# Performance work log

Hardware: AMD Instinct MI355X
Metric: run time of the kernel (lower is better)

## Reference

```python
import jax, jax.numpy as jnp
import numpy as np

EPS = 1e-6
K_STEPS = 4
USE_GATING = True


def layer_norm(x, gamma, beta):
    mu = jnp.mean(x, axis=-1, keepdims=True)
    var = jnp.mean(jnp.square(x - mu), axis=-1, keepdims=True)
    return (x - mu) * jax.lax.rsqrt(var + EPS) * gamma + beta


def setup_inputs() -> dict:
    key = jax.random.key(0)
    B, L, D, H = 4, 4096, 2048, 8192
    ks = jax.random.split(key, 16)
    s = 0.02
    return {
        "x": jax.random.normal(ks[0], (B, L, D), dtype=jnp.float32),
        "in_gamma": jnp.ones((D,), jnp.float32),
        "in_beta": jnp.zeros((D,), jnp.float32),
        "agg_w": jax.random.normal(ks[1], (D, D), jnp.float32) * s,
        "agg_b": jnp.zeros((D,), jnp.float32),
        "pn_gamma": jnp.ones((D,), jnp.float32),
        "pn_beta": jnp.zeros((D,), jnp.float32),
        "d1_w": jax.random.normal(ks[2], (D, H), jnp.float32) * s,
        "d1_b": jnp.zeros((H,), jnp.float32),
        "d2_w": jax.random.normal(ks[3], (H, D), jnp.float32) * s,
        "d2_b": jnp.zeros((D,), jnp.float32),
        "bc_w": jax.random.normal(ks[4], (D, D), jnp.float32) * s,
        "bc_b": jnp.zeros((D,), jnp.float32),
        "gate_w": jax.random.normal(ks[5], (D, D), jnp.float32) * s,
        "gate_b": jnp.zeros((D,), jnp.float32),
        "out_gamma": jnp.ones((D,), jnp.float32),
        "out_beta": jnp.zeros((D,), jnp.float32),
    }


def reference(x, in_gamma, in_beta, agg_w, agg_b, pn_gamma, pn_beta,
              d1_w, d1_b, d2_w, d2_b, bc_w, bc_b, gate_w, gate_b,
              out_gamma, out_beta):
    # Input norm over the full sequence, then extract last-position summary.
    x_norm = layer_norm(x, in_gamma, in_beta)              # [B, L, D]
    thought = x_norm[:, -1, :] @ agg_w + agg_b             # [B, D]

    # Iterative pre-norm MLP thought refinement (fixed small k -> unrolled).
    for _ in range(K_STEPS):
        t = layer_norm(thought, pn_gamma, pn_beta)
        t = jax.nn.gelu(t @ d1_w + d1_b, approximate=False)
        thought = thought + (t @ d2_w + d2_b)

    # Broadcast refined thought back to every position.
    broadcast = (thought @ bc_w + bc_b)[:, None, :]        # [B, 1, D]

    if USE_GATING:
        gate = jax.nn.sigmoid(x @ gate_w + gate_b)         # [B, L, D]
        out = x + gate * broadcast
    else:
        out = x + broadcast
    return layer_norm(out, out_gamma, out_beta)
```

## Files before the change

### kernel.cpp

```cpp
#include <hip/hip_runtime.h>
#include <stdint.h>

typedef __attribute__((ext_vector_type(8))) short short8;
typedef __attribute__((ext_vector_type(4))) float f32x4;
typedef __attribute__((ext_vector_type(4))) unsigned short us4;

__device__ inline unsigned short f2bf(float f) {
    unsigned u = __float_as_uint(f);
    u = (u + 0x7FFFu + ((u >> 16) & 1u)) >> 16;
    return (unsigned short)u;
}

__device__ inline void gload_lds16(const unsigned short* g, const unsigned short* l) {
    __builtin_amdgcn_global_load_lds(
        (const __attribute__((address_space(1))) unsigned int*)(g),
        (__attribute__((address_space(3))) unsigned int*)(l),
        16, 0, 0);
}

__global__ __launch_bounds__(256) void cvt_x_kernel(const float* __restrict__ in,
                                                    unsigned short* __restrict__ out, int n4) {
    int i = blockIdx.x * 256 + threadIdx.x;
    if (i >= n4) return;
    float4 v = reinterpret_cast<const float4*>(in)[i];
    us4 o = { f2bf(v.x), f2bf(v.y), f2bf(v.z), f2bf(v.w) };
    reinterpret_cast<us4*>(out)[i] = o;
}

__global__ __launch_bounds__(256) void transpose_w_kernel(const float* __restrict__ W,
                                                          unsigned short* __restrict__ WT,
                                                          int K, int N) {
    __shared__ float tile[32][33];
    int bn = blockIdx.x * 32;
    int bk = blockIdx.y * 32;
    int tx = threadIdx.x & 31;
    int ty = threadIdx.x >> 5;
#pragma unroll
    for (int j = 0; j < 32; j += 8)
        tile[ty + j][tx] = W[(long long)(bk + ty + j) * N + bn + tx];
    __syncthreads();
#pragma unroll
    for (int j = 0; j < 32; j += 8)
        WT[(long long)(bn + ty + j) * K + bk + tx] = f2bf(tile[tx][ty + j]);
}

__device__ inline void block_reduce2(float& s, float& q) {
#pragma unroll
    for (int o = 32; o > 0; o >>= 1) {
        s += __shfl_xor(s, o, 64);
        q += __shfl_xor(q, o, 64);
    }
    __shared__ float sh[8];
    int w = threadIdx.x >> 6;
    if ((threadIdx.x & 63) == 0) { sh[w] = s; sh[4 + w] = q; }
    __syncthreads();
    s = (sh[0] + sh[1]) + (sh[2] + sh[3]);
    q = (sh[4] + sh[5]) + (sh[6] + sh[7]);
}

__global__ __launch_bounds__(256) void ln_rows_kernel(const float* __restrict__ in, long long in_stride,
                                                      float* __restrict__ out, long long out_stride,
                                                      const float* __restrict__ gamma,
                                                      const float* __restrict__ beta) {
    const float* p = in + (long long)blockIdx.x * in_stride;
    float* q = out + (long long)blockIdx.x * out_stride;
    int t = threadIdx.x;
    float4 a = reinterpret_cast<const float4*>(p)[t];
    float4 c = reinterpret_cast<const float4*>(p)[t + 256];
    float s  = (a.x + a.y) + (a.z + a.w) + (c.x + c.y) + (c.z + c.w);
    float ss = a.x*a.x + a.y*a.y + a.z*a.z + a.w*a.w
             + c.x*c.x + c.y*c.y + c.z*c.z + c.w*c.w;
    block_reduce2(s, ss);
    const float inv = 1.0f / 2048.0f;
    float mu = s * inv;
    float var = ss * inv - mu * mu;
    float rs = rsqrtf(var + 1e-6f);
    float4 g0 = reinterpret_cast<const float4*>(gamma)[t];
    float4 g1 = reinterpret_cast<const float4*>(gamma)[t + 256];
    float4 b0 = reinterpret_cast<const float4*>(beta)[t];
    float4 b1 = reinterpret_cast<const float4*>(beta)[t + 256];
    float4 o0, o1;
    o0.x = (a.x - mu) * rs * g0.x + b0.x;
    o0.y = (a.y - mu) * rs * g0.y + b0.y;
    o0.z = (a.z - mu) * rs * g0.z + b0.z;
    o0.w = (a.w - mu) * rs * g0.w + b0.w;
    o1.x = (c.x - mu) * rs * g1.x + b1.x;
    o1.y = (c.y - mu) * rs * g1.y + b1.y;
    o1.z = (c.z - mu) * rs * g1.z + b1.z;
    o1.w = (c.w - mu) * rs * g1.w + b1.w;
    reinterpret_cast<float4*>(q)[t] = o0;
    reinterpret_cast<float4*>(q)[t + 256] = o1;
}

__global__ __launch_bounds__(256) void gelu_kernel(float* __restrict__ h, int n) {
    int i = blockIdx.x * 256 + threadIdx.x;
    if (i < n) {
        float v = h[i];
        h[i] = 0.5f * v * (1.0f + erff(v * 0.70710678118654752f));
    }
}

__global__ __launch_bounds__(256) void gemv4_kernel(const float* __restrict__ in,
                                                    const float* __restrict__ W,
                                                    const float* __restrict__ bias,
                                                    float* __restrict__ out,
                                                    int K, int N, int KC) {
    const int n4 = blockIdx.x * 256 + threadIdx.x;
    const int n = n4 * 4;
    const int k0 = blockIdx.y * KC;
    const float4* W4 = reinterpret_cast<const float4*>(W);
    const float* i0 = in;
    const float* i1 = in + K;
    const float* i2 = in + 2 * K;
    const float* i3 = in + 3 * K;
    float4 a0 = {0.f, 0.f, 0.f, 0.f}, a1 = a0, a2 = a0, a3 = a0;
#pragma unroll 4
    for (int k = k0; k < k0 + KC; ++k) {
        float4 w = W4[((long long)k * N + n) >> 2];
        float c0 = i0[k], c1 = i1[k], c2 = i2[k], c3 = i3[k];
        a0.x = fmaf(c0, w.x, a0.x); a0.y = fmaf(c0, w.y, a0.y);
        a0.z = fmaf(c0, w.z, a0.z); a0.w = fmaf(c0, w.w, a0.w);
        a1.x = fmaf(c1, w.x, a1.x); a1.y = fmaf(c1, w.y, a1.y);
        a1.z = fmaf(c1, w.z, a1.z); a1.w = fmaf(c1, w.w, a1.w);
        a2.x = fmaf(c2, w.x, a2.x); a2.y = fmaf(c2, w.y, a2.y);
        a2.z = fmaf(c2, w.z, a2.z); a2.w = fmaf(c2, w.w, a2.w);
        a3.x = fmaf(c3, w.x, a3.x); a3.y = fmaf(c3, w.y, a3.y);
        a3.z = fmaf(c3, w.z, a3.z); a3.w = fmaf(c3, w.w, a3.w);
    }
    if (blockIdx.y == 0) {
        float4 b = reinterpret_cast<const float4*>(bias)[n4];
        a0.x += b.x; a0.y += b.y; a0.z += b.z; a0.w += b.w;
        a1.x += b.x; a1.y += b.y; a1.z += b.z; a1.w += b.w;
        a2.x += b.x; a2.y += b.y; a2.z += b.z; a2.w += b.w;
        a3.x += b.x; a3.y += b.y; a3.z += b.z; a3.w += b.w;
    }
    atomicAdd(&out[n + 0], a0.x); atomicAdd(&out[n + 1], a0.y);
    atomicAdd(&out[n + 2], a0.z); atomicAdd(&out[n + 3], a0.w);
    atomicAdd(&out[N + n + 0], a1.x); atomicAdd(&out[N + n + 1], a1.y);
    atomicAdd(&out[N + n + 2], a1.z); atomicAdd(&out[N + n + 3], a1.w);
    atomicAdd(&out[2 * N + n + 0], a2.x); atomicAdd(&out[2 * N + n + 1], a2.y);
    atomicAdd(&out[2 * N + n + 2], a2.z); atomicAdd(&out[2 * N + n + 3], a2.w);
    atomicAdd(&out[3 * N + n + 0], a3.x); atomicAdd(&out[3 * N + n + 1], a3.y);
    atomicAdd(&out[3 * N + n + 2], a3.z); atomicAdd(&out[3 * N + n + 3], a3.w);
}

#define BK 64
__global__ __launch_bounds__(512, 2) void gate_gemm_kernel(const unsigned short* __restrict__ A,
                                                           const unsigned short* __restrict__ BT,
                                                           const float* __restrict__ xf,
                                                           const float* __restrict__ gate_b,
                                                           const float* __restrict__ bcast,
                                                           float* __restrict__ pre,
                                                           int M, int N, int K) {
    extern __shared__ unsigned short lds[];
    const int tid = threadIdx.x;
    const int lane = tid & 63;
    const int wave = tid >> 6;
    const int wm = wave >> 2;
    const int wn = wave & 3;
    const int bm0 = blockIdx.x * 256;
    const int bn0 = blockIdx.y * 256;
    const int NT = K / BK;

    const int ch0 = wave * 64 + lane;
    const int ch1 = 512 + wave * 64 + lane;
    const int r0 = ch0 >> 3, c0s = (ch0 & 7) ^ (r0 & 7);
    const int r1 = ch1 >> 3, c1s = (ch1 & 7) ^ (r1 & 7);
    const int srcoff0 = r0 * K + c0s * 8;
    const int srcoff1 = r1 * K + c1s * 8;
    const int ldso0 = ch0 * 8;
    const int ldso1 = ch1 * 8;

    const unsigned short* Abase = A + (long long)bm0 * K;
    const unsigned short* Bbase = BT + (long long)bn0 * K;

#define STAGE_A(buf, h, t)  do { \
        const unsigned short* g = Abase + (h) * 128 * K + (t) * BK; \
        const unsigned short* d = &lds[(buf) * 16384 + (h) * 8192]; \
        gload_lds16(g + srcoff0, d + ldso0); \
        gload_lds16(g + srcoff1, d + ldso1); } while (0)
#define STAGE_B(buf, h, t)  do { \
        const unsigned short* g = Bbase + (h) * 128 * K + (t) * BK; \
        const unsigned short* d = &lds[32768 + (buf) * 16384 + (h) * 8192]; \
        gload_lds16(g + srcoff0, d + ldso0); \
        gload_lds16(g + srcoff1, d + ldso1); } while (0)

    f32x4 acc[8][4];
#pragma unroll
    for (int i = 0; i < 8; ++i)
#pragma unroll
        for (int j = 0; j < 4; ++j)
#pragma unroll
            for (int r = 0; r < 4; ++r) acc[i][j][r] = 0.f;

    const int r16 = lane & 15, kq = lane >> 4;
    const int bwrow = (wn & 1) * 64;

    STAGE_A(0, 0, 0); STAGE_A(0, 1, 0);
    STAGE_B(0, 0, 0); STAGE_B(0, 1, 0);
    asm volatile("s_waitcnt vmcnt(0)" ::: "memory");
    __builtin_amdgcn_s_barrier();

    for (int t = 0; t < NT; ++t) {
        const int p = t & 1;
        const int u = t + 1;
        const int a_base = p * 16384 + wm * 8192;
        const int b_base = 32768 + p * 16384 + (wn >> 1) * 8192;

#pragma unroll
        for (int q = 0; q < 4; ++q) {
            const int mh = (q >> 1) * 4;
            const int nh = (q & 1) * 2;
            short8 af[4][2], bf[2][2];
#pragma unroll
            for (int mi = 0; mi < 4; ++mi) {
                const int rl = (mh + mi) * 16 + r16;
#pragma unroll
                for (int kk = 0; kk < 2; ++kk)
                    af[mi][kk] = *reinterpret_cast<const short8*>(
                        &lds[a_base + rl * 64 + (((kk << 2) | kq) ^ (rl & 7)) * 8]);
            }
#pragma unroll
            for (int ni = 0; ni < 2; ++ni) {
                const int rl = bwrow + (nh + ni) * 16 + r16;
#pragma unroll
                for (int kk = 0; kk < 2; ++kk)
                    bf[ni][kk] = *reinterpret_cast<const short8*>(
                        &lds[b_base + rl * 64 + (((kk << 2) | kq) ^ (rl & 7)) * 8]);
            }
            if (q == 0 && u < NT) { STAGE_A(1 - p, 0, u); STAGE_A(1 - p, 1, u); }
            if (q == 1 && u < NT) { STAGE_B(1 - p, 0, u); STAGE_B(1 - p, 1, u); }
            __builtin_amdgcn_s_barrier();
            __builtin_amdgcn_s_setprio(1);
#pragma unroll
            for (int mi = 0; mi < 4; ++mi)
#pragma unroll
                for (int ni = 0; ni < 2; ++ni)
#pragma unroll
                    for (int kk = 0; kk < 2; ++kk)
                        acc[mh + mi][nh + ni] = __builtin_amdgcn_mfma_f32_16x16x32_bf16(
                            af[mi][kk], bf[ni][kk], acc[mh + mi][nh + ni], 0, 0, 0);
            __builtin_amdgcn_s_setprio(0);
            if (q == 3) asm volatile("s_waitcnt vmcnt(0)" ::: "memory");
            __builtin_amdgcn_s_barrier();
        }
    }

    const int bnum = bm0 >> 12;
    const float* bc_row = bcast + (long long)bnum * N;
#pragma unroll
    for (int mi = 0; mi < 8; ++mi) {
        const int row = bm0 + wm * 128 + mi * 16 + kq * 4;
#pragma unroll
        for (int ni = 0; ni < 4; ++ni) {
            const int col = bn0 + wn * 64 + ni * 16 + r16;
            const float gb = gate_b[col];
            const float bc = bc_row[col];
#pragma unroll
            for (int r = 0; r < 4; ++r) {
                const long long off = (long long)(row + r) * N + col;
                const float v = acc[mi][ni][r] + gb;
                const float g = 1.0f / (1.0f + __expf(-v));
                pre[off] = xf[off] + g * bc;
            }
        }
    }
}
#undef STAGE_A
#undef STAGE_B

extern "C" void kernel_launch(void* const* d_in, const int* in_sizes, int n_in,
                              void* d_out, int out_size, void* d_ws, size_t ws_size,
                              hipStream_t stream) {
    const float* x         = (const float*)d_in[0];
    const float* in_gamma  = (const float*)d_in[1];
    const float* in_beta   = (const float*)d_in[2];
    const float* agg_w     = (const float*)d_in[3];
    const float* agg_b     = (const float*)d_in[4];
    const float* pn_gamma  = (const float*)d_in[5];
    const float* pn_beta   = (const float*)d_in[6];
    const float* d1_w      = (const float*)d_in[7];
    const float* d1_b      = (const float*)d_in[8];
    const float* d2_w      = (const float*)d_in[9];
    const float* d2_b      = (const float*)d_in[10];
    const float* bc_w      = (const float*)d_in[11];
    const float* bc_b      = (const float*)d_in[12];
    const float* gate_w    = (const float*)d_in[13];
    const float* gate_b    = (const float*)d_in[14];
    const float* out_gamma = (const float*)d_in[15];
    const float* out_beta  = (const float*)d_in[16];

    const int B = 4, L = 4096, D = 2048, H = 8192;
    const int M = B * L;
    float* out = (float*)d_out;

    char* ws = (char*)d_ws;
    unsigned short* xb  = (unsigned short*)ws;
    unsigned short* gwT = (unsigned short*)(ws + 67108864);
    float* tln   = (float*)(ws + 75497472);
    float* tbuf  = tln + 4 * D;
    float* hbuf  = tbuf + 4 * D;
    float* bcast = hbuf + 4 * H;

    static bool attr_done = false;
    if (!attr_done) {
        hipFuncSetAttribute((const void*)gate_gemm_kernel,
                            hipFuncAttributeMaxDynamicSharedMemorySize, 131072);
        attr_done = true;
    }

    ln_rows_kernel<<<dim3(B), dim3(256), 0, stream>>>(
        x + (long long)(L - 1) * D, (long long)L * D, tln, (long long)D, in_gamma, in_beta);
    hipMemsetAsync(tbuf, 0, 4 * D * sizeof(float), stream);
    gemv4_kernel<<<dim3(D / 1024, 64), dim3(256), 0, stream>>>(tln, agg_w, agg_b, tbuf, D, D, 32);

    for (int s = 0; s < 4; ++s) {
        ln_rows_kernel<<<dim3(B), dim3(256), 0, stream>>>(
            tbuf, (long long)D, tln, (long long)D, pn_gamma, pn_beta);
        hipMemsetAsync(hbuf, 0, 4 * H * sizeof(float), stream);
        gemv4_kernel<<<dim3(H / 1024, 32), dim3(256), 0, stream>>>(tln, d1_w, d1_b, hbuf, D, H, 64);
        gelu_kernel<<<dim3(B * H / 256), dim3(256), 0, stream>>>(hbuf, B * H);
        gemv4_kernel<<<dim3(D / 1024, 128), dim3(256), 0, stream>>>(hbuf, d2_w, d2_b, tbuf, H, D, 64);
    }
    hipMemsetAsync(bcast, 0, 4 * D * sizeof(float), stream);
    gemv4_kernel<<<dim3(D / 1024, 64), dim3(256), 0, stream>>>(tbuf, bc_w, bc_b, bcast, D, D, 32);

    cvt_x_kernel<<<dim3((M * D / 4) / 256), dim3(256), 0, stream>>>(x, xb, M * D / 4);
    transpose_w_kernel<<<dim3(D / 32, D / 32), dim3(256), 0, stream>>>(gate_w, gwT, D, D);

    gate_gemm_kernel<<<dim3(M / 256, D / 256), dim3(512), 131072, stream>>>(
        xb, gwT, x, gate_b, bcast, out, M, D, D);

    ln_rows_kernel<<<dim3(M), dim3(256), 0, stream>>>(
        out, (long long)D, out, (long long)D, out_gamma, out_beta);
}
```

Before: 559.1 us.

## Fuse layernorm/GELU into GEMV prologue and switch gate GEMM to 32x32 MFMA

Folds the per-row layernorm and the GELU into a templated GEMV kernel that stages normalized or activated inputs in LDS, which removes separate ln and gelu launches from the serial refinement chain. Each GEMV block redundantly recomputes row statistics over the full K. Separately, the large gate GEMM switches from 16x16x32 to 32x32x16 bf16 MFMA with a reorganized fragment layout and epilogue. A barrier is also added in block_reduce2 so the shared scratch can be reused safely across repeated calls.

```diff
diff --git a/kernel.cpp b/kernel.cpp
--- a/kernel.cpp
+++ b/kernel.cpp
@@ -3,12 +3,17 @@
 
 typedef __attribute__((ext_vector_type(8))) short short8;
 typedef __attribute__((ext_vector_type(4))) float f32x4;
+typedef __attribute__((ext_vector_type(16))) float f32x16;
 typedef __attribute__((ext_vector_type(4))) unsigned short us4;
 
 __device__ inline unsigned short f2bf(float f) {
     unsigned u = __float_as_uint(f);
     u = (u + 0x7FFFu + ((u >> 16) & 1u)) >> 16;
     return (unsigned short)u;
+}
+
+__device__ inline float gelu_f(float v) {
+    return 0.5f * v * (1.0f + erff(v * 0.70710678118654752f));
 }
 
 __device__ inline void gload_lds16(const unsigned short* g, const unsigned short* l) {
@@ -51,6 +56,7 @@
         q += __shfl_xor(q, o, 64);
     }
     __shared__ float sh[8];
+    __syncthreads();
     int w = threadIdx.x >> 6;
     if ((threadIdx.x & 63) == 0) { sh[w] = s; sh[4 + w] = q; }
     __syncthreads();
@@ -92,32 +98,48 @@
     reinterpret_cast<float4*>(q)[t + 256] = o1;
 }
 
-__global__ __launch_bounds__(256) void gelu_kernel(float* __restrict__ h, int n) {
-    int i = blockIdx.x * 256 + threadIdx.x;
-    if (i < n) {
-        float v = h[i];
-        h[i] = 0.5f * v * (1.0f + erff(v * 0.70710678118654752f));
-    }
-}
-
-__global__ __launch_bounds__(256) void gemv4_kernel(const float* __restrict__ in,
-                                                    const float* __restrict__ W,
-                                                    const float* __restrict__ bias,
-                                                    float* __restrict__ out,
-                                                    int K, int N, int KC) {
-    const int n4 = blockIdx.x * 256 + threadIdx.x;
+template<int MODE>
+__global__ __launch_bounds__(256) void gemv4f_kernel(const float* __restrict__ src, long long sstride,
+                                                     const float* __restrict__ gamma,
+                                                     const float* __restrict__ beta,
+                                                     const float* __restrict__ W,
+                                                     const float* __restrict__ bias,
+                                                     float* __restrict__ out,
+                                                     int K, int N, int KC) {
+    __shared__ float sA[4][128];
+    const int tid = threadIdx.x;
+    const int k0 = blockIdx.y * KC;
+
+    float mu[4], rsd[4];
+    if (MODE == 1) {
+#pragma unroll
+        for (int r = 0; r < 4; ++r) {
+            const float* p = src + r * sstride;
+            float s = 0.f, q = 0.f;
+            for (int k = tid; k < K; k += 256) { float v = p[k]; s += v; q += v * v; }
+            block_reduce2(s, q);
+            float m = s / K;
+            mu[r] = m;
+            rsd[r] = rsqrtf(q / K - m * m + 1e-6f);
+        }
+    }
+    for (int idx = tid; idx < 4 * KC; idx += 256) {
+        int r = idx / KC, k = idx - r * KC;
+        float v = src[r * sstride + k0 + k];
+        if (MODE == 1) v = (v - mu[r]) * rsd[r] * gamma[k0 + k] + beta[k0 + k];
+        if (MODE == 2) v = gelu_f(v);
+        sA[r][k] = v;
+    }
+    __syncthreads();
+
+    const int n4 = blockIdx.x * 256 + tid;
     const int n = n4 * 4;
-    const int k0 = blockIdx.y * KC;
     const float4* W4 = reinterpret_cast<const float4*>(W);
-    const float* i0 = in;
-    const float* i1 = in + K;
-    const float* i2 = in + 2 * K;
-    const float* i3 = in + 3 * K;
     float4 a0 = {0.f, 0.f, 0.f, 0.f}, a1 = a0, a2 = a0, a3 = a0;
 #pragma unroll 4
-    for (int k = k0; k < k0 + KC; ++k) {
-        float4 w = W4[((long long)k * N + n) >> 2];
-        float c0 = i0[k], c1 = i1[k], c2 = i2[k], c3 = i3[k];
+    for (int k = 0; k < KC; ++k) {
+        float4 w = W4[((long long)(k0 + k) * N + n) >> 2];
+        float c0 = sA[0][k], c1 = sA[1][k], c2 = sA[2][k], c3 = sA[3][k];
         a0.x = fmaf(c0, w.x, a0.x); a0.y = fmaf(c0, w.y, a0.y);
         a0.z = fmaf(c0, w.z, a0.z); a0.w = fmaf(c0, w.w, a0.w);
         a1.x = fmaf(c1, w.x, a1.x); a1.y = fmaf(c1, w.y, a1.y);
@@ -185,16 +207,16 @@
         gload_lds16(g + srcoff0, d + ldso0); \
         gload_lds16(g + srcoff1, d + ldso1); } while (0)
 
-    f32x4 acc[8][4];
-#pragma unroll
-    for (int i = 0; i < 8; ++i)
-#pragma unroll
-        for (int j = 0; j < 4; ++j)
-#pragma unroll
-            for (int r = 0; r < 4; ++r) acc[i][j][r] = 0.f;
-
-    const int r16 = lane & 15, kq = lane >> 4;
-    const int bwrow = (wn & 1) * 64;
+    f32x16 acc[4][2];
+#pragma unroll
+    for (int i = 0; i < 4; ++i)
+#pragma unroll
+        for (int j = 0; j < 2; ++j)
+#pragma unroll
+            for (int r = 0; r < 16; ++r) acc[i][j][r] = 0.f;
+
+    const int l31 = lane & 31, kh = lane >> 5;
+    const int brow0 = (wn & 1) * 64;
 
     STAGE_A(0, 0, 0); STAGE_A(0, 1, 0);
     STAGE_B(0, 0, 0); STAGE_B(0, 1, 0);
@@ -208,40 +230,42 @@
         const int b_base = 32768 + p * 16384 + (wn >> 1) * 8192;
 
 #pragma unroll
-        for (int q = 0; q < 4; ++q) {
-            const int mh = (q >> 1) * 4;
-            const int nh = (q & 1) * 2;
+        for (int ph = 0; ph < 2; ++ph) {
             short8 af[4][2], bf[2][2];
 #pragma unroll
-            for (int mi = 0; mi < 4; ++mi) {
-                const int rl = (mh + mi) * 16 + r16;
-#pragma unroll
-                for (int kk = 0; kk < 2; ++kk)
-                    af[mi][kk] = *reinterpret_cast<const short8*>(
-                        &lds[a_base + rl * 64 + (((kk << 2) | kq) ^ (rl & 7)) * 8]);
+            for (int mt = 0; mt < 4; ++mt) {
+                const int rl = mt * 32 + l31;
+#pragma unroll
+                for (int s = 0; s < 2; ++s) {
+                    const int c = (ph * 2 + s) * 2 + kh;
+                    af[mt][s] = *reinterpret_cast<const short8*>(
+                        &lds[a_base + rl * 64 + ((c ^ (rl & 7)) * 8)]);
+                }
             }
 #pragma unroll
-            for (int ni = 0; ni < 2; ++ni) {
-                const int rl = bwrow + (nh + ni) * 16 + r16;
-#pragma unroll
-                for (int kk = 0; kk < 2; ++kk)
-                    bf[ni][kk] = *reinterpret_cast<const short8*>(
-                        &lds[b_base + rl * 64 + (((kk << 2) | kq) ^ (rl & 7)) * 8]);
+            for (int nt = 0; nt < 2; ++nt) {
+                const int rl = brow0 + nt * 32 + l31;
+#pragma unroll
+                for (int s = 0; s < 2; ++s) {
+                    const int c = (ph * 2 + s) * 2 + kh;
+                    bf[nt][s] = *reinterpret_cast<const short8*>(
+                        &lds[b_base + rl * 64 + ((c ^ (rl & 7)) * 8)]);
+                }
             }
-            if (q == 0 && u < NT) { STAGE_A(1 - p, 0, u); STAGE_A(1 - p, 1, u); }
-            if (q == 1 && u < NT) { STAGE_B(1 - p, 0, u); STAGE_B(1 - p, 1, u); }
+            if (ph == 0 && u < NT) { STAGE_A(1 - p, 0, u); STAGE_A(1 - p, 1, u); }
+            if (ph == 1 && u < NT) { STAGE_B(1 - p, 0, u); STAGE_B(1 - p, 1, u); }
             __builtin_amdgcn_s_barrier();
             __builtin_amdgcn_s_setprio(1);
 #pragma unroll
-            for (int mi = 0; mi < 4; ++mi)
-#pragma unroll
-                for (int ni = 0; ni < 2; ++ni)
-#pragma unroll
-                    for (int kk = 0; kk < 2; ++kk)
-                        acc[mh + mi][nh + ni] = __builtin_amdgcn_mfma_f32_16x16x32_bf16(
-                            af[mi][kk], bf[ni][kk], acc[mh + mi][nh + ni], 0, 0, 0);
+            for (int s = 0; s < 2; ++s)
+#pragma unroll
+                for (int mt = 0; mt < 4; ++mt)
+#pragma unroll
+                    for (int nt = 0; nt < 2; ++nt)
+                        acc[mt][nt] = __builtin_amdgcn_mfma_f32_32x32x16_bf16(
+                            af[mt][s], bf[nt][s], acc[mt][nt], 0, 0, 0);
             __builtin_amdgcn_s_setprio(0);
-            if (q == 3) asm volatile("s_waitcnt vmcnt(0)" ::: "memory");
+            if (ph == 1) asm volatile("s_waitcnt vmcnt(0)" ::: "memory");
             __builtin_amdgcn_s_barrier();
         }
     }
@@ -249,17 +273,18 @@
     const int bnum = bm0 >> 12;
     const float* bc_row = bcast + (long long)bnum * N;
 #pragma unroll
-    for (int mi = 0; mi < 8; ++mi) {
-        const int row = bm0 + wm * 128 + mi * 16 + kq * 4;
-#pragma unroll
-        for (int ni = 0; ni < 4; ++ni) {
-            const int col = bn0 + wn * 64 + ni * 16 + r16;
+    for (int mt = 0; mt < 4; ++mt) {
+        const int row0e = bm0 + wm * 128 + mt * 32 + 4 * kh;
+#pragma unroll
+        for (int nt = 0; nt < 2; ++nt) {
+            const int col = bn0 + wn * 64 + nt * 32 + l31;
             const float gb = gate_b[col];
             const float bc = bc_row[col];
 #pragma unroll
-            for (int r = 0; r < 4; ++r) {
-                const long long off = (long long)(row + r) * N + col;
-                const float v = acc[mi][ni][r] + gb;
+            for (int r = 0; r < 16; ++r) {
+                const int row = row0e + (r & 3) + 8 * (r >> 2);
+                const long long off = (long long)row * N + col;
+                const float v = acc[mt][nt][r] + gb;
                 const float g = 1.0f / (1.0f + __expf(-v));
                 pre[off] = xf[off] + g * bc;
             }
@@ -297,8 +322,7 @@
     char* ws = (char*)d_ws;
     unsigned short* xb  = (unsigned short*)ws;
     unsigned short* gwT = (unsigned short*)(ws + 67108864);
-    float* tln   = (float*)(ws + 75497472);
-    float* tbuf  = tln + 4 * D;
+    float* tbuf  = (float*)(ws + 75497472);
     float* hbuf  = tbuf + 4 * D;
     float* bcast = hbuf + 4 * H;
 
@@ -309,21 +333,21 @@
         attr_done = true;
     }
 
-    ln_rows_kernel<<<dim3(B), dim3(256), 0, stream>>>(
-        x + (long long)(L - 1) * D, (long long)L * D, tln, (long long)D, in_gamma, in_beta);
     hipMemsetAsync(tbuf, 0, 4 * D * sizeof(float), stream);
-    gemv4_kernel<<<dim3(D / 1024, 64), dim3(256), 0, stream>>>(tln, agg_w, agg_b, tbuf, D, D, 32);
+    gemv4f_kernel<1><<<dim3(D / 1024, 64), dim3(256), 0, stream>>>(
+        x + (long long)(L - 1) * D, (long long)L * D, in_gamma, in_beta,
+        agg_w, agg_b, tbuf, D, D, 32);
 
     for (int s = 0; s < 4; ++s) {
-        ln_rows_kernel<<<dim3(B), dim3(256), 0, stream>>>(
-            tbuf, (long long)D, tln, (long long)D, pn_gamma, pn_beta);
         hipMemsetAsync(hbuf, 0, 4 * H * sizeof(float), stream);
-        gemv4_kernel<<<dim3(H / 1024, 32), dim3(256), 0, stream>>>(tln, d1_w, d1_b, hbuf, D, H, 64);
-        gelu_kernel<<<dim3(B * H / 256), dim3(256), 0, stream>>>(hbuf, B * H);
-        gemv4_kernel<<<dim3(D / 1024, 128), dim3(256), 0, stream>>>(hbuf, d2_w, d2_b, tbuf, H, D, 64);
+        gemv4f_kernel<1><<<dim3(H / 1024, 32), dim3(256), 0, stream>>>(
+            tbuf, (long long)D, pn_gamma, pn_beta, d1_w, d1_b, hbuf, D, H, 64);
+        gemv4f_kernel<2><<<dim3(D / 1024, 128), dim3(256), 0, stream>>>(
+            hbuf, (long long)H, nullptr, nullptr, d2_w, d2_b, tbuf, H, D, 64);
     }
     hipMemsetAsync(bcast, 0, 4 * D * sizeof(float), stream);
-    gemv4_kernel<<<dim3(D / 1024, 64), dim3(256), 0, stream>>>(tbuf, bc_w, bc_b, bcast, D, D, 32);
+    gemv4f_kernel<0><<<dim3(D / 1024, 64), dim3(256), 0, stream>>>(
+        tbuf, (long long)D, nullptr, nullptr, bc_w, bc_b, bcast, D, D, 32);
 
     cvt_x_kernel<<<dim3((M * D / 4) / 256), dim3(256), 0, stream>>>(x, xb, M * D / 4);
     transpose_w_kernel<<<dim3(D / 32, D / 32), dim3(256), 0, stream>>>(gate_w, gwT, D, D);
```

Result: slower. 574.5 us (+2.8%).
